# Optimization experiments

Hardware: AMD Instinct MI355X
Metric: run time of the kernel (lower is better)

The kernel has to match this reference:

```python
import jax, jax.numpy as jnp
import numpy as np

B, T, C, H = 4, 1024, 1024, 16
D = C // H  # head_size = 64
F = 4 * C   # ffn hidden


def _ln(x, g, b, eps=1e-5):
    m = x.mean(-1, keepdims=True)
    v = ((x - m) ** 2).mean(-1, keepdims=True)
    return (x - m) * jax.lax.rsqrt(v + eps) * g + b


def setup_inputs() -> dict:
    key = jax.random.key(0)
    ks = jax.random.split(key, 12)
    w = lambda k, shape: (jax.random.normal(k, shape, jnp.float32) * 0.02)
    return dict(
        x=jax.random.normal(ks[0], (B, T, C), jnp.float32),
        padding_mask=(jax.random.randint(ks[1], (B, T), 0, 2) == 1),
        Wq=w(ks[2], (H, C, D)),
        Wk=w(ks[3], (H, C, D)),
        Wv=w(ks[4], (H, C, D)),
        Wo=w(ks[5], (C, C)),
        bo=jnp.zeros((C,), jnp.float32),
        ln1_g=jnp.ones((C,), jnp.float32),
        ln1_b=jnp.zeros((C,), jnp.float32),
        ln2_g=jnp.ones((C,), jnp.float32),
        ln2_b=jnp.zeros((C,), jnp.float32),
        W1=w(ks[6], (C, F)),
        b1=jnp.zeros((F,), jnp.float32),
        W2=w(ks[7], (F, C)),
        b2=jnp.zeros((C,), jnp.float32),
    )


def reference(x, padding_mask, Wq, Wk, Wv, Wo, bo, ln1_g, ln1_b, ln2_g, ln2_b, W1, b1, W2, b2):
    Bn, Tn, Cn = x.shape
    h = _ln(x, ln1_g, ln1_b)
    # per-head q/k/v projections (no bias), vectorized over heads
    q = jnp.einsum('btc,hcd->bhtd', h, Wq)
    k = jnp.einsum('btc,hcd->bhtd', h, Wk)
    v = jnp.einsum('btc,hcd->bhtd', h, Wv)
    # NOTE: faithful to source, scale uses full n_embed C, not head_size
    wei = jnp.einsum('bhtd,bhsd->bhts', q, k) * (Cn ** -0.5)
    causal = jnp.tril(jnp.ones((Tn, Tn), bool))
    wei = jnp.where(causal[None, None], wei, -jnp.inf)
    # padding mask applied after causal, with -1e9 (as in source)
    wei = jnp.where(padding_mask[:, None, None, :], jnp.float32(-1e9), wei)
    att = jax.nn.softmax(wei, axis=-1)  # dropout is identity (eval)
    out = jnp.einsum('bhts,bhsd->bhtd', att, v)
    out = out.transpose(0, 2, 1, 3).reshape(Bn, Tn, Cn)  # concat heads
    out = out @ Wo + bo  # output projection
    # NOTE: no residual connections in the source TransformerBlock
    h2 = _ln(out, ln2_g, ln2_b)
    return jax.nn.relu(h2 @ W1 + b1) @ W2 + b2
```

## Files before the change

kernel.cpp:

```cpp
#include <hip/hip_runtime.h>
#include <hip/hip_bf16.h>
#include <math.h>

constexpr int kB = 4;
constexpr int kT = 1024;
constexpr int kC = 1024;
constexpr int kH = 16;
constexpr int kD = 64;
constexpr int kF = 4096;
constexpr int kBT = kB * kT;
constexpr int kSplit = 2;

typedef __attribute__((ext_vector_type(8))) short short8;
typedef __attribute__((ext_vector_type(4))) float f32x4;

__device__ __forceinline__ unsigned short f2bf(float f) {
    __hip_bfloat16 h = __float2bfloat16(f);
    return __builtin_bit_cast(unsigned short, h);
}
__device__ __forceinline__ float bf2f(unsigned short u) {
    return __bfloat162float(__builtin_bit_cast(__hip_bfloat16, u));
}


__global__ __launch_bounds__(256) void ln_bf16_kernel(const float* __restrict__ x,
                                                      const float* __restrict__ g,
                                                      const float* __restrict__ bta,
                                                      unsigned short* __restrict__ out) {
    int row = blockIdx.x;
    int t = threadIdx.x;
    float4 xv = ((const float4*)(x + (size_t)row * kC))[t];
    float s  = xv.x + xv.y + xv.z + xv.w;
    float sq = xv.x * xv.x + xv.y * xv.y + xv.z * xv.z + xv.w * xv.w;
    #pragma unroll
    for (int off = 32; off; off >>= 1) {
        s  += __shfl_xor(s, off);
        sq += __shfl_xor(sq, off);
    }
    __shared__ float sb[8];
    int wid = t >> 6, lane = t & 63;
    if (lane == 0) { sb[wid] = s; sb[4 + wid] = sq; }
    __syncthreads();
    s  = sb[0] + sb[1] + sb[2] + sb[3];
    sq = sb[4] + sb[5] + sb[6] + sb[7];
    float mean = s * (1.0f / kC);
    float var  = sq * (1.0f / kC) - mean * mean;
    float rs = rsqrtf(var + 1e-5f);
    float4 gv = ((const float4*)g)[t];
    float4 bv = ((const float4*)bta)[t];
    ushort4 o;
    o.x = f2bf((xv.x - mean) * rs * gv.x + bv.x);
    o.y = f2bf((xv.y - mean) * rs * gv.y + bv.y);
    o.z = f2bf((xv.z - mean) * rs * gv.z + bv.z);
    o.w = f2bf((xv.w - mean) * rs * gv.w + bv.w);
    *(ushort4*)(out + (size_t)row * kC + t * 4) = o;
}

__global__ __launch_bounds__(256) void transpose_w_kernel(const float* __restrict__ src,
                                                          unsigned short* __restrict__ dst,
                                                          int R, int C) {
    __shared__ float tile[64][65];
    src += (size_t)blockIdx.z * R * C;
    dst += (size_t)blockIdx.z * R * C;
    int r0 = blockIdx.x * 64, c0 = blockIdx.y * 64;
    int tid = threadIdx.x;
    int tr = tid >> 4, tc4 = (tid & 15) * 4;
    #pragma unroll
    for (int p = 0; p < 4; p++) {
        float4 v = *(const float4*)(src + (size_t)(r0 + tr + p * 16) * C + c0 + tc4);
        tile[tr + p * 16][tc4 + 0] = v.x;
        tile[tr + p * 16][tc4 + 1] = v.y;
        tile[tr + p * 16][tc4 + 2] = v.z;
        tile[tr + p * 16][tc4 + 3] = v.w;
    }
    __syncthreads();
    #pragma unroll
    for (int p = 0; p < 4; p++) {
        int c = tr + p * 16;
        ushort4 o;
        o.x = f2bf(tile[tc4 + 0][c]);
        o.y = f2bf(tile[tc4 + 1][c]);
        o.z = f2bf(tile[tc4 + 2][c]);
        o.w = f2bf(tile[tc4 + 3][c]);
        *(ushort4*)(dst + (size_t)(c0 + c) * R + r0 + tc4) = o;
    }
}

__global__ __launch_bounds__(256) void transpose_v_kernel(const unsigned short* __restrict__ qkv,
                                                          unsigned short* __restrict__ vt) {
    __shared__ unsigned short tile[64][68];
    int bh = blockIdx.y, b = bh >> 4, h = bh & 15;
    int t0 = blockIdx.x * 64;
    int tid = threadIdx.x;
    int tr = tid >> 4, tc4 = (tid & 15) * 4;
    #pragma unroll
    for (int p = 0; p < 4; p++) {
        int t = t0 + tr + p * 16;
        ushort4 v = *(const ushort4*)(qkv + ((size_t)(b * kT + t)) * 3072 + 2048 + h * 64 + tc4);
        *(ushort4*)&tile[tr + p * 16][tc4] = v;
    }
    __syncthreads();
    #pragma unroll
    for (int p = 0; p < 4; p++) {
        int d = tr + p * 16;
        ushort4 o;
        o.x = tile[tc4 + 0][d];
        o.y = tile[tc4 + 1][d];
        o.z = tile[tc4 + 2][d];
        o.w = tile[tc4 + 3][d];
        *(ushort4*)(vt + ((size_t)(bh * 64 + d)) * kT + t0 + tc4) = o;
    }
}

__global__ __launch_bounds__(256) void padscan_kernel(const int* __restrict__ pad,
                                                      int* __restrict__ npad,
                                                      int* __restrict__ fu) {
    int b = blockIdx.x, tid = threadIdx.x;
    int cnt = 0, f = kT;
    for (int t = tid; t < kT; t += 256) {
        int p = pad[b * kT + t];
        cnt += p;
        if (!p) f = min(f, t);
    }
    __shared__ int sc[256], sf[256];
    sc[tid] = cnt; sf[tid] = f;
    __syncthreads();
    for (int o = 128; o; o >>= 1) {
        if (tid < o) { sc[tid] += sc[tid + o]; sf[tid] = min(sf[tid], sf[tid + o]); }
        __syncthreads();
    }
    if (tid == 0) { npad[b] = sc[0]; fu[b] = sf[0]; }
}

__global__ __launch_bounds__(256) void meanv_kernel(const unsigned short* __restrict__ vt,
                                                    const int* __restrict__ pad,
                                                    const int* __restrict__ npad,
                                                    float* __restrict__ meanv) {
    int bh = blockIdx.x, b = bh >> 4;
    int tid = threadIdx.x, d = tid >> 2, seg = tid & 3;
    const unsigned short* row = vt + ((size_t)bh * 64 + d) * kT + seg * 256;
    const int* pr = pad + b * kT + seg * 256;
    float s = 0.f;
    for (int t = 0; t < 256; ++t)
        if (pr[t]) s += bf2f(row[t]);
    __shared__ float red[256];
    red[tid] = s;
    __syncthreads();
    if (seg == 0) {
        float tot = red[tid] + red[tid + 1] + red[tid + 2] + red[tid + 3];
        int np = npad[b];
        meanv[bh * 64 + d] = np > 0 ? tot / (float)np : 0.f;
    }
}

__global__ __launch_bounds__(256) void fixup_kernel(unsigned short* __restrict__ attnb,
                                                    const float* __restrict__ meanv,
                                                    const int* __restrict__ fu) {
    int b = blockIdx.x, tid = threadIdx.x;
    int f = fu[b];
    int c = tid * 4;
    ushort4 u;
    u.x = f2bf(meanv[b * kC + c + 0]);
    u.y = f2bf(meanv[b * kC + c + 1]);
    u.z = f2bf(meanv[b * kC + c + 2]);
    u.w = f2bf(meanv[b * kC + c + 3]);
    for (int t = 0; t < f; ++t)
        *(ushort4*)(attnb + ((size_t)(b * kT + t)) * kC + c) = u;
}

__global__ __launch_bounds__(256) void attn_partial(const unsigned short* __restrict__ qkv,
                                                    const unsigned short* __restrict__ vt,
                                                    const int* __restrict__ pad,
                                                    unsigned short* __restrict__ Opart,
                                                    float* __restrict__ Mpart,
                                                    float* __restrict__ Lpart) {
    __shared__ __align__(16) unsigned short Ks[64][72];
    __shared__ __align__(16) unsigned short Vs[64][72];
    __shared__ __align__(16) unsigned short Ps[4][16][72];
    const int tid = threadIdx.x;
    const int x = blockIdx.x, bh = blockIdx.y, j = blockIdx.z;
    const int b = bh >> 4, h = bh & 15;
    const int wv = tid >> 6, lane = tid & 63;
    const int lm = lane & 15, lk = lane >> 4;
    const int srow = tid >> 2, scol = (tid & 3) * 16;

    const int qrow = x * 64 + wv * 16 + lm;
    const size_t qoff = ((size_t)(b * kT + qrow)) * 3072 + h * 64 + lk * 8;
    short8 bq0 = *(const short8*)(qkv + qoff);
    short8 bq1 = *(const short8*)(qkv + qoff + 32);

    const unsigned short* kbase = qkv + ((size_t)(b * kT + srow)) * 3072 + 1024 + h * 64 + scol;
    const unsigned short* vbase = vt + ((size_t)(bh * 64 + srow)) * kT + scol;

    f32x4 o[4];
    #pragma unroll
    for (int dt = 0; dt < 4; dt++) o[dt] = (f32x4){0.f, 0.f, 0.f, 0.f};
    float m_i = -__builtin_inff(), l_i = 0.f;

    short8 kp0 = *(const short8*)(kbase + (size_t)(j * 64) * 3072);
    short8 kp1 = *(const short8*)(kbase + (size_t)(j * 64) * 3072 + 8);
    short8 vp0 = *(const short8*)(vbase + j * 64);
    short8 vp1 = *(const short8*)(vbase + j * 64 + 8);

    for (int c = j; c <= x; c += kSplit) {
        const int s0 = c * 64;
        *(short8*)&Ks[srow][scol] = kp0;
        *(short8*)&Ks[srow][scol + 8] = kp1;
        *(short8*)&Vs[srow][scol] = vp0;
        *(short8*)&Vs[srow][scol + 8] = vp1;
        __syncthreads();
        if (c + kSplit <= x) {
            const int sn = (c + kSplit) * 64;
            kp0 = *(const short8*)(kbase + (size_t)sn * 3072);
            kp1 = *(const short8*)(kbase + (size_t)sn * 3072 + 8);
            vp0 = *(const short8*)(vbase + sn);
            vp1 = *(const short8*)(vbase + sn + 8);
        }
        float xs[16];
        #pragma unroll
        for (int g = 0; g < 4; g++) {
            short8 ka0 = *(const short8*)&Ks[g * 16 + lm][lk * 8];
            short8 ka1 = *(const short8*)&Ks[g * 16 + lm][32 + lk * 8];
            f32x4 sc = (f32x4){0.f, 0.f, 0.f, 0.f};
            sc = __builtin_amdgcn_mfma_f32_16x16x32_bf16(ka0, bq0, sc, 0, 0, 0);
            sc = __builtin_amdgcn_mfma_f32_16x16x32_bf16(ka1, bq1, sc, 0, 0, 0);
            int sbase = s0 + g * 16 + lk * 4;
            int4 pv = *(const int4*)(pad + b * kT + sbase);
            int pa[4] = {pv.x, pv.y, pv.z, pv.w};
            #pragma unroll
            for (int r = 0; r < 4; r++) {
                float v = sc[r] * 0.03125f;
                if (sbase + r > qrow) v = -__builtin_inff();
                if (pa[r]) v = -1e9f;
                xs[g * 4 + r] = v;
            }
        }
        float mt = xs[0];
        #pragma unroll
        for (int i = 1; i < 16; i++) mt = fmaxf(mt, xs[i]);
        mt = fmaxf(mt, __shfl_xor(mt, 16));
        mt = fmaxf(mt, __shfl_xor(mt, 32));
        float mn = fmaxf(m_i, mt);
        float alpha = __expf(m_i - mn);
        float p[16], rs = 0.f;
        #pragma unroll
        for (int i = 0; i < 16; i++) { p[i] = __expf(xs[i] - mn); rs += p[i]; }
        rs += __shfl_xor(rs, 16);
        rs += __shfl_xor(rs, 32);
        l_i = l_i * alpha + rs;
        m_i = mn;
        #pragma unroll
        for (int g = 0; g < 4; g++) {
            ushort4 u;
            u.x = f2bf(p[g * 4 + 0]); u.y = f2bf(p[g * 4 + 1]);
            u.z = f2bf(p[g * 4 + 2]); u.w = f2bf(p[g * 4 + 3]);
            *(ushort4*)&Ps[wv][lm][g * 16 + lk * 4] = u;
        }
        float ar0 = __shfl(alpha, lk * 4 + 0);
        float ar1 = __shfl(alpha, lk * 4 + 1);
        float ar2 = __shfl(alpha, lk * 4 + 2);
        float ar3 = __shfl(alpha, lk * 4 + 3);
        #pragma unroll
        for (int dt = 0; dt < 4; dt++) {
            o[dt][0] *= ar0; o[dt][1] *= ar1; o[dt][2] *= ar2; o[dt][3] *= ar3;
        }
        short8 ap0 = *(const short8*)&Ps[wv][lm][lk * 8];
        short8 ap1 = *(const short8*)&Ps[wv][lm][32 + lk * 8];
        #pragma unroll
        for (int dt = 0; dt < 4; dt++) {
            short8 bv0 = *(const short8*)&Vs[dt * 16 + lm][lk * 8];
            short8 bv1 = *(const short8*)&Vs[dt * 16 + lm][32 + lk * 8];
            o[dt] = __builtin_amdgcn_mfma_f32_16x16x32_bf16(ap0, bv0, o[dt], 0, 0, 0);
            o[dt] = __builtin_amdgcn_mfma_f32_16x16x32_bf16(ap1, bv1, o[dt], 0, 0, 0);
        }
        __syncthreads();
    }
    const size_t base = ((size_t)(bh * kSplit + j)) * kT;
    if (lk == 0) {
        Mpart[base + qrow] = m_i;
        Lpart[base + qrow] = l_i;
    }
    #pragma unroll
    for (int dt = 0; dt < 4; dt++)
        #pragma unroll
        for (int r = 0; r < 4; r++) {
            int q = x * 64 + wv * 16 + lk * 4 + r;
            Opart[(base + q) * kD + dt * 16 + lm] = f2bf(o[dt][r]);
        }
}

__global__ __launch_bounds__(256) void attn_merge(const unsigned short* __restrict__ Opart,
                                                  const float* __restrict__ Mpart,
                                                  const float* __restrict__ Lpart,
                                                  unsigned short* __restrict__ attnb) {
    const int xq = blockIdx.x, bh = blockIdx.y;
    const int b = bh >> 4, h = bh & 15;
    const int tid = threadIdx.x;
    const int qo = tid >> 4, d4 = (tid & 15) * 4;
    #pragma unroll
    for (int pass = 0; pass < 4; pass++) {
        int q = xq * 64 + pass * 16 + qo;
        float m[kSplit], l[kSplit];
        float mstar = -__builtin_inff();
        #pragma unroll
        for (int jj = 0; jj < kSplit; jj++) {
            size_t base = ((size_t)(bh * kSplit + jj)) * kT + q;
            m[jj] = Mpart[base];
            l[jj] = Lpart[base];
            if (l[jj] > 0.f) mstar = fmaxf(mstar, m[jj]);
        }
        float acc0 = 0.f, acc1 = 0.f, acc2 = 0.f, acc3 = 0.f, L = 0.f;
        #pragma unroll
        for (int jj = 0; jj < kSplit; jj++) {
            if (l[jj] > 0.f) {
                float wgt = __expf(m[jj] - mstar);
                L += wgt * l[jj];
                ushort4 ov = *(const ushort4*)&Opart[(((size_t)(bh * kSplit + jj)) * kT + q) * kD + d4];
                acc0 += wgt * bf2f(ov.x);
                acc1 += wgt * bf2f(ov.y);
                acc2 += wgt * bf2f(ov.z);
                acc3 += wgt * bf2f(ov.w);
            }
        }
        float inv = 1.0f / L;
        ushort4 r;
        r.x = f2bf(acc0 * inv); r.y = f2bf(acc1 * inv);
        r.z = f2bf(acc2 * inv); r.w = f2bf(acc3 * inv);
        *(ushort4*)&attnb[((size_t)(b * kT + q)) * kC + h * 64 + d4] = r;
    }
}

template<int TM, int TN>
__global__ __launch_bounds__(256) void gemm_bt(const unsigned short* __restrict__ A,
                                               const unsigned short* __restrict__ Bt,
                                               const float* __restrict__ bias,
                                               float* __restrict__ Cf,
                                               unsigned short* __restrict__ Cb,
                                               int N, int K, int relu) {
    constexpr int AI = TM / 32, BJ = TN / 32;
    constexpr int TPRA = 256 / TM, TPRB = 256 / TN;
    constexpr int ACH = 64 / TPRA / 8, BCH = 64 / TPRB / 8;
    __shared__ __align__(16) unsigned short As[TM][72];
    __shared__ __align__(16) unsigned short Bs[TN][72];
    const int tid = threadIdx.x;
    const int wv = tid >> 6, lane = tid & 63;
    const int lm = lane & 15, lk = lane >> 4;
    const int arow = tid / TPRA, acb = (tid % TPRA) * (64 / TPRA);
    const int brow = tid / TPRB, bcb = (tid % TPRB) * (64 / TPRB);
    const int bm = blockIdx.y * TM, bn = blockIdx.x * TN;
    const int wm = (wv >> 1) * (TM / 2), wn = (wv & 1) * (TN / 2);
    f32x4 acc[AI][BJ];
    #pragma unroll
    for (int i = 0; i < AI; i++)
        #pragma unroll
        for (int j = 0; j < BJ; j++) acc[i][j] = (f32x4){0.f, 0.f, 0.f, 0.f};

    const unsigned short* Ap = A + (size_t)(bm + arow) * K + acb;
    const unsigned short* Bp = Bt + (size_t)(bn + brow) * K + bcb;
    short8 rA[ACH], rB[BCH];
    #pragma unroll
    for (int i = 0; i < ACH; i++) rA[i] = *(const short8*)(Ap + i * 8);
    #pragma unroll
    for (int i = 0; i < BCH; i++) rB[i] = *(const short8*)(Bp + i * 8);

    for (int k0 = 0; k0 < K; k0 += 64) {
        #pragma unroll
        for (int i = 0; i < ACH; i++)
            *(short8*)&As[arow][acb + i * 8] = rA[i];
        #pragma unroll
        for (int i = 0; i < BCH; i++)
            *(short8*)&Bs[brow][bcb + i * 8] = rB[i];
        __syncthreads();
        if (k0 + 64 < K) {
            #pragma unroll
            for (int i = 0; i < ACH; i++) rA[i] = *(const short8*)(Ap + k0 + 64 + i * 8);
            #pragma unroll
            for (int i = 0; i < BCH; i++) rB[i] = *(const short8*)(Bp + k0 + 64 + i * 8);
        }
        #pragma unroll
        for (int kk = 0; kk < 2; kk++) {
            short8 a[AI], bfr[BJ];
            #pragma unroll
            for (int i = 0; i < AI; i++)
                a[i] = *(const short8*)&As[wm + i * 16 + lm][kk * 32 + lk * 8];
            #pragma unroll
            for (int j = 0; j < BJ; j++)
                bfr[j] = *(const short8*)&Bs[wn + j * 16 + lm][kk * 32 + lk * 8];
            #pragma unroll
            for (int i = 0; i < AI; i++)
                #pragma unroll
                for (int j = 0; j < BJ; j++)
                    acc[i][j] = __builtin_amdgcn_mfma_f32_16x16x32_bf16(a[i], bfr[j], acc[i][j], 0, 0, 0);
        }
        __syncthreads();
    }
    #pragma unroll
    for (int j = 0; j < BJ; j++) {
        int col = bn + wn + j * 16 + lm;
        float bj = bias ? bias[col] : 0.f;
        #pragma unroll
        for (int i = 0; i < AI; i++) {
            #pragma unroll
            for (int r = 0; r < 4; r++) {
                int row = bm + wm + i * 16 + lk * 4 + r;
                float v = acc[i][j][r] + bj;
                if (relu) v = fmaxf(v, 0.f);
                if (Cf) Cf[(size_t)row * N + col] = v;
                else    Cb[(size_t)row * N + col] = f2bf(v);
            }
        }
    }
}

extern "C" void kernel_launch(void* const* d_in, const int* in_sizes, int n_in,
                              void* d_out, int out_size, void* d_ws, size_t ws_size,
                              hipStream_t stream) {
    (void)in_sizes; (void)n_in; (void)out_size; (void)ws_size;
    const float* x    = (const float*)d_in[0];
    const int*   pad  = (const int*)d_in[1];
    const float* Wq   = (const float*)d_in[2];
    const float* Wk   = (const float*)d_in[3];
    const float* Wv   = (const float*)d_in[4];
    const float* Wo   = (const float*)d_in[5];
    const float* bo   = (const float*)d_in[6];
    const float* ln1g = (const float*)d_in[7];
    const float* ln1b = (const float*)d_in[8];
    const float* ln2g = (const float*)d_in[9];
    const float* ln2b = (const float*)d_in[10];
    const float* W1   = (const float*)d_in[11];
    const float* b1   = (const float*)d_in[12];
    const float* W2   = (const float*)d_in[13];
    const float* b2   = (const float*)d_in[14];
    float* out = (float*)d_out;
    char* w = (char*)d_ws;

    constexpr size_t MB = 1024 * 1024;
    unsigned short* qkv   = (unsigned short*)(w + 0);
    float*          proj  = (float*)(w + 0);
    unsigned short* h2    = (unsigned short*)(w + 16 * MB);
    unsigned short* vt    = (unsigned short*)(w + 24 * MB);
    unsigned short* attnb = (unsigned short*)(w + 32 * MB);
    unsigned short* w1t   = (unsigned short*)(w + 40 * MB);
    unsigned short* w2t   = (unsigned short*)(w + 48 * MB);
    unsigned short* wot   = (unsigned short*)(w + 56 * MB);
    float*          meanv = (float*)(w + 58 * MB);
    int*            npad  = (int*)(w + 58 * MB + 65536);
    int*            fu    = (int*)(w + 58 * MB + 65536 + 64);
    unsigned short* h     = (unsigned short*)(w + 59 * MB);
    unsigned short* wqkvt = (unsigned short*)(w + 67 * MB);
    unsigned short* Opart = (unsigned short*)(w + 59 * MB);
    unsigned short* ffn1  = (unsigned short*)(w + 59 * MB);
    float*          Mpart = (float*)(w + 91 * MB);
    float*          Lpart = (float*)(w + 91 * MB + 512 * 1024);

    transpose_w_kernel<<<dim3(16, 1, 16), 256, 0, stream>>>(Wq, wqkvt,               kC, kD);
    transpose_w_kernel<<<dim3(16, 1, 16), 256, 0, stream>>>(Wk, wqkvt + 1024 * 1024, kC, kD);
    transpose_w_kernel<<<dim3(16, 1, 16), 256, 0, stream>>>(Wv, wqkvt + 2048 * 1024, kC, kD);
    transpose_w_kernel<<<dim3(16, 16, 1), 256, 0, stream>>>(Wo, wot, kC, kC);
    transpose_w_kernel<<<dim3(16, 64, 1), 256, 0, stream>>>(W1, w1t, kC, kF);
    transpose_w_kernel<<<dim3(64, 16, 1), 256, 0, stream>>>(W2, w2t, kF, kC);

    ln_bf16_kernel<<<kBT, 256, 0, stream>>>(x, ln1g, ln1b, h);
    gemm_bt<128, 128><<<dim3(24, 32), 256, 0, stream>>>(h, wqkvt, nullptr, nullptr, qkv,
                                                        3072, kC, 0);
    transpose_v_kernel<<<dim3(16, 64), 256, 0, stream>>>(qkv, vt);
    padscan_kernel<<<kB, 256, 0, stream>>>(pad, npad, fu);
    meanv_kernel<<<kB * kH, 256, 0, stream>>>(vt, pad, npad, meanv);
    attn_partial<<<dim3(16, 64, kSplit), 256, 0, stream>>>(qkv, vt, pad, Opart, Mpart, Lpart);
    attn_merge<<<dim3(16, 64), 256, 0, stream>>>(Opart, Mpart, Lpart, attnb);
    fixup_kernel<<<kB, 256, 0, stream>>>(attnb, meanv, fu);
    gemm_bt<128, 64><<<dim3(16, 32), 256, 0, stream>>>(attnb, wot, bo, proj, nullptr,
                                                       kC, kC, 0);
    ln_bf16_kernel<<<kBT, 256, 0, stream>>>(proj, ln2g, ln2b, h2);
    gemm_bt<128, 128><<<dim3(32, 32), 256, 0, stream>>>(h2, w1t, b1, nullptr, ffn1,
                                                        kF, kC, 1);
    gemm_bt<128, 64><<<dim3(16, 32), 256, 0, stream>>>(ffn1, w2t, b2, out, nullptr,
                                                       kC, kF, 0);
}
```

Baseline: 414.2 us.

## Merge weight transposes, fold padscan/fixup into meanv/merge, double-buffer GEMM LDS

All six weight-transpose launches become one kernel with a flat block index. The pad scan moves into meanv_kernel, and the fully-padded-row fixup moves into attn_merge, which cuts three launches and a serial fixup kernel. The GEMM now uses a K-tile of 32 with double-buffered LDS and one barrier per step, so loads overlap MFMA. In exchange, each GEMM step does half as much MFMA work per barrier, and meanv repeats the pad reduction in every head block.

```diff
diff --git a/kernel.cpp b/kernel.cpp
--- a/kernel.cpp
+++ b/kernel.cpp
@@ -56,13 +56,10 @@
     *(ushort4*)(out + (size_t)row * kC + t * 4) = o;
 }
 
-__global__ __launch_bounds__(256) void transpose_w_kernel(const float* __restrict__ src,
-                                                          unsigned short* __restrict__ dst,
-                                                          int R, int C) {
-    __shared__ float tile[64][65];
-    src += (size_t)blockIdx.z * R * C;
-    dst += (size_t)blockIdx.z * R * C;
-    int r0 = blockIdx.x * 64, c0 = blockIdx.y * 64;
+__device__ __forceinline__ void tile_tr(const float* __restrict__ src,
+                                        unsigned short* __restrict__ dst,
+                                        int R, int C, int r0, int c0,
+                                        float (*tile)[65]) {
     int tid = threadIdx.x;
     int tr = tid >> 4, tc4 = (tid & 15) * 4;
     #pragma unroll
@@ -86,6 +83,36 @@
     }
 }
 
+__global__ __launch_bounds__(256) void transpose_all(const float* __restrict__ Wq,
+                                                     const float* __restrict__ Wk,
+                                                     const float* __restrict__ Wv,
+                                                     const float* __restrict__ Wo,
+                                                     const float* __restrict__ W1,
+                                                     const float* __restrict__ W2,
+                                                     unsigned short* __restrict__ wqkvt,
+                                                     unsigned short* __restrict__ wot,
+                                                     unsigned short* __restrict__ w1t,
+                                                     unsigned short* __restrict__ w2t) {
+    __shared__ float tile[64][65];
+    int id = blockIdx.x;
+    if (id < 768) {
+        int wsel = id >> 8, t = id & 255;
+        int z = t >> 4, xq = t & 15;
+        const float* s = (wsel == 0 ? Wq : wsel == 1 ? Wk : Wv) + (size_t)z * 65536;
+        tile_tr(s, wqkvt + (size_t)wsel * 1048576 + (size_t)z * 65536,
+                1024, 64, xq * 64, 0, tile);
+    } else if (id < 1024) {
+        int t = id - 768;
+        tile_tr(Wo, wot, 1024, 1024, (t & 15) * 64, (t >> 4) * 64, tile);
+    } else if (id < 2048) {
+        int t = id - 1024;
+        tile_tr(W1, w1t, 1024, 4096, (t & 15) * 64, (t >> 4) * 64, tile);
+    } else {
+        int t = id - 2048;
+        tile_tr(W2, w2t, 4096, 1024, (t & 63) * 64, (t >> 6) * 64, tile);
+    }
+}
+
 __global__ __launch_bounds__(256) void transpose_v_kernel(const unsigned short* __restrict__ qkv,
                                                           unsigned short* __restrict__ vt) {
     __shared__ unsigned short tile[64][68];
@@ -112,60 +139,53 @@
     }
 }
 
-__global__ __launch_bounds__(256) void padscan_kernel(const int* __restrict__ pad,
-                                                      int* __restrict__ npad,
-                                                      int* __restrict__ fu) {
-    int b = blockIdx.x, tid = threadIdx.x;
-    int cnt = 0, f = kT;
-    for (int t = tid; t < kT; t += 256) {
-        int p = pad[b * kT + t];
-        cnt += p;
-        if (!p) f = min(f, t);
-    }
-    __shared__ int sc[256], sf[256];
-    sc[tid] = cnt; sf[tid] = f;
-    __syncthreads();
-    for (int o = 128; o; o >>= 1) {
-        if (tid < o) { sc[tid] += sc[tid + o]; sf[tid] = min(sf[tid], sf[tid + o]); }
-        __syncthreads();
-    }
-    if (tid == 0) { npad[b] = sc[0]; fu[b] = sf[0]; }
-}
-
 __global__ __launch_bounds__(256) void meanv_kernel(const unsigned short* __restrict__ vt,
                                                     const int* __restrict__ pad,
-                                                    const int* __restrict__ npad,
-                                                    float* __restrict__ meanv) {
+                                                    float* __restrict__ meanv,
+                                                    int* __restrict__ fu) {
     int bh = blockIdx.x, b = bh >> 4;
-    int tid = threadIdx.x, d = tid >> 2, seg = tid & 3;
+    int tid = threadIdx.x;
+    __shared__ char padc[kT];
+    __shared__ int ri[256];
+    __shared__ float rf[256];
+    int4 pv = *(const int4*)(pad + b * kT + tid * 4);
+    padc[tid * 4 + 0] = (char)pv.x;
+    padc[tid * 4 + 1] = (char)pv.y;
+    padc[tid * 4 + 2] = (char)pv.z;
+    padc[tid * 4 + 3] = (char)pv.w;
+    int cnt = pv.x + pv.y + pv.z + pv.w;
+    int f = kT;
+    if (!pv.w) f = tid * 4 + 3;
+    if (!pv.z) f = tid * 4 + 2;
+    if (!pv.y) f = tid * 4 + 1;
+    if (!pv.x) f = tid * 4 + 0;
+    ri[tid] = f;
+    __syncthreads();
+    for (int o = 128; o; o >>= 1) {
+        if (tid < o) ri[tid] = min(ri[tid], ri[tid + o]);
+        __syncthreads();
+    }
+    int fu_s = ri[0];
+    __syncthreads();
+    ri[tid] = cnt;
+    __syncthreads();
+    for (int o = 128; o; o >>= 1) {
+        if (tid < o) ri[tid] += ri[tid + o];
+        __syncthreads();
+    }
+    int np = ri[0];
+    int d = tid >> 2, seg = tid & 3;
     const unsigned short* row = vt + ((size_t)bh * 64 + d) * kT + seg * 256;
-    const int* pr = pad + b * kT + seg * 256;
     float s = 0.f;
     for (int t = 0; t < 256; ++t)
-        if (pr[t]) s += bf2f(row[t]);
-    __shared__ float red[256];
-    red[tid] = s;
+        if (padc[seg * 256 + t]) s += bf2f(row[t]);
+    rf[tid] = s;
     __syncthreads();
     if (seg == 0) {
-        float tot = red[tid] + red[tid + 1] + red[tid + 2] + red[tid + 3];
-        int np = npad[b];
+        float tot = rf[tid] + rf[tid + 1] + rf[tid + 2] + rf[tid + 3];
         meanv[bh * 64 + d] = np > 0 ? tot / (float)np : 0.f;
     }
-}
-
-__global__ __launch_bounds__(256) void fixup_kernel(unsigned short* __restrict__ attnb,
-                                                    const float* __restrict__ meanv,
-                                                    const int* __restrict__ fu) {
-    int b = blockIdx.x, tid = threadIdx.x;
-    int f = fu[b];
-    int c = tid * 4;
-    ushort4 u;
-    u.x = f2bf(meanv[b * kC + c + 0]);
-    u.y = f2bf(meanv[b * kC + c + 1]);
-    u.z = f2bf(meanv[b * kC + c + 2]);
-    u.w = f2bf(meanv[b * kC + c + 3]);
-    for (int t = 0; t < f; ++t)
-        *(ushort4*)(attnb + ((size_t)(b * kT + t)) * kC + c) = u;
+    if (tid == 0 && (bh & 15) == 0) fu[b] = fu_s;
 }
 
 __global__ __launch_bounds__(256) void attn_partial(const unsigned short* __restrict__ qkv,
@@ -292,40 +312,50 @@
 __global__ __launch_bounds__(256) void attn_merge(const unsigned short* __restrict__ Opart,
                                                   const float* __restrict__ Mpart,
                                                   const float* __restrict__ Lpart,
+                                                  const float* __restrict__ meanv,
+                                                  const int* __restrict__ fu,
                                                   unsigned short* __restrict__ attnb) {
     const int xq = blockIdx.x, bh = blockIdx.y;
     const int b = bh >> 4, h = bh & 15;
     const int tid = threadIdx.x;
     const int qo = tid >> 4, d4 = (tid & 15) * 4;
+    const int f = fu[b];
     #pragma unroll
     for (int pass = 0; pass < 4; pass++) {
         int q = xq * 64 + pass * 16 + qo;
-        float m[kSplit], l[kSplit];
-        float mstar = -__builtin_inff();
-        #pragma unroll
-        for (int jj = 0; jj < kSplit; jj++) {
-            size_t base = ((size_t)(bh * kSplit + jj)) * kT + q;
-            m[jj] = Mpart[base];
-            l[jj] = Lpart[base];
-            if (l[jj] > 0.f) mstar = fmaxf(mstar, m[jj]);
-        }
-        float acc0 = 0.f, acc1 = 0.f, acc2 = 0.f, acc3 = 0.f, L = 0.f;
-        #pragma unroll
-        for (int jj = 0; jj < kSplit; jj++) {
-            if (l[jj] > 0.f) {
-                float wgt = __expf(m[jj] - mstar);
-                L += wgt * l[jj];
-                ushort4 ov = *(const ushort4*)&Opart[(((size_t)(bh * kSplit + jj)) * kT + q) * kD + d4];
-                acc0 += wgt * bf2f(ov.x);
-                acc1 += wgt * bf2f(ov.y);
-                acc2 += wgt * bf2f(ov.z);
-                acc3 += wgt * bf2f(ov.w);
+        ushort4 r;
+        if (q < f) {
+            r.x = f2bf(meanv[bh * 64 + d4 + 0]);
+            r.y = f2bf(meanv[bh * 64 + d4 + 1]);
+            r.z = f2bf(meanv[bh * 64 + d4 + 2]);
+            r.w = f2bf(meanv[bh * 64 + d4 + 3]);
+        } else {
+            float m[kSplit], l[kSplit];
+            float mstar = -__builtin_inff();
+            #pragma unroll
+            for (int jj = 0; jj < kSplit; jj++) {
+                size_t base = ((size_t)(bh * kSplit + jj)) * kT + q;
+                m[jj] = Mpart[base];
+                l[jj] = Lpart[base];
+                if (l[jj] > 0.f) mstar = fmaxf(mstar, m[jj]);
             }
-        }
-        float inv = 1.0f / L;
-        ushort4 r;
-        r.x = f2bf(acc0 * inv); r.y = f2bf(acc1 * inv);
-        r.z = f2bf(acc2 * inv); r.w = f2bf(acc3 * inv);
+            float acc0 = 0.f, acc1 = 0.f, acc2 = 0.f, acc3 = 0.f, L = 0.f;
+            #pragma unroll
+            for (int jj = 0; jj < kSplit; jj++) {
+                if (l[jj] > 0.f) {
+                    float wgt = __expf(m[jj] - mstar);
+                    L += wgt * l[jj];
+                    ushort4 ov = *(const ushort4*)&Opart[(((size_t)(bh * kSplit + jj)) * kT + q) * kD + d4];
+                    acc0 += wgt * bf2f(ov.x);
+                    acc1 += wgt * bf2f(ov.y);
+                    acc2 += wgt * bf2f(ov.z);
+                    acc3 += wgt * bf2f(ov.w);
+                }
+            }
+            float inv = 1.0f / L;
+            r.x = f2bf(acc0 * inv); r.y = f2bf(acc1 * inv);
+            r.z = f2bf(acc2 * inv); r.w = f2bf(acc3 * inv);
+        }
         *(ushort4*)&attnb[((size_t)(b * kT + q)) * kC + h * 64 + d4] = r;
     }
 }
@@ -339,14 +369,14 @@
                                                int N, int K, int relu) {
     constexpr int AI = TM / 32, BJ = TN / 32;
     constexpr int TPRA = 256 / TM, TPRB = 256 / TN;
-    constexpr int ACH = 64 / TPRA / 8, BCH = 64 / TPRB / 8;
-    __shared__ __align__(16) unsigned short As[TM][72];
-    __shared__ __align__(16) unsigned short Bs[TN][72];
+    constexpr int ACH = 32 / TPRA / 8, BCH = 32 / TPRB / 8;
+    __shared__ __align__(16) unsigned short As[2][TM][40];
+    __shared__ __align__(16) unsigned short Bs[2][TN][40];
     const int tid = threadIdx.x;
     const int wv = tid >> 6, lane = tid & 63;
     const int lm = lane & 15, lk = lane >> 4;
-    const int arow = tid / TPRA, acb = (tid % TPRA) * (64 / TPRA);
-    const int brow = tid / TPRB, bcb = (tid % TPRB) * (64 / TPRB);
+    const int arow = tid / TPRA, acb = (tid % TPRA) * (32 / TPRA);
+    const int brow = tid / TPRB, bcb = (tid % TPRB) * (32 / TPRB);
     const int bm = blockIdx.y * TM, bn = blockIdx.x * TN;
     const int wm = (wv >> 1) * (TM / 2), wn = (wv & 1) * (TN / 2);
     f32x4 acc[AI][BJ];
@@ -362,35 +392,38 @@
     for (int i = 0; i < ACH; i++) rA[i] = *(const short8*)(Ap + i * 8);
     #pragma unroll
     for (int i = 0; i < BCH; i++) rB[i] = *(const short8*)(Bp + i * 8);
-
-    for (int k0 = 0; k0 < K; k0 += 64) {
-        #pragma unroll
-        for (int i = 0; i < ACH; i++)
-            *(short8*)&As[arow][acb + i * 8] = rA[i];
-        #pragma unroll
-        for (int i = 0; i < BCH; i++)
-            *(short8*)&Bs[brow][bcb + i * 8] = rB[i];
-        __syncthreads();
-        if (k0 + 64 < K) {
-            #pragma unroll
-            for (int i = 0; i < ACH; i++) rA[i] = *(const short8*)(Ap + k0 + 64 + i * 8);
-            #pragma unroll
-            for (int i = 0; i < BCH; i++) rB[i] = *(const short8*)(Bp + k0 + 64 + i * 8);
-        }
-        #pragma unroll
-        for (int kk = 0; kk < 2; kk++) {
-            short8 a[AI], bfr[BJ];
-            #pragma unroll
-            for (int i = 0; i < AI; i++)
-                a[i] = *(const short8*)&As[wm + i * 16 + lm][kk * 32 + lk * 8];
+    #pragma unroll
+    for (int i = 0; i < ACH; i++) *(short8*)&As[0][arow][acb + i * 8] = rA[i];
+    #pragma unroll
+    for (int i = 0; i < BCH; i++) *(short8*)&Bs[0][brow][bcb + i * 8] = rB[i];
+    __syncthreads();
+
+    for (int k0 = 0; k0 < K; k0 += 32) {
+        const int cur = (k0 >> 5) & 1;
+        const bool more = (k0 + 32 < K);
+        if (more) {
+            #pragma unroll
+            for (int i = 0; i < ACH; i++) rA[i] = *(const short8*)(Ap + k0 + 32 + i * 8);
+            #pragma unroll
+            for (int i = 0; i < BCH; i++) rB[i] = *(const short8*)(Bp + k0 + 32 + i * 8);
+        }
+        short8 a[AI], bfr[BJ];
+        #pragma unroll
+        for (int i = 0; i < AI; i++)
+            a[i] = *(const short8*)&As[cur][wm + i * 16 + lm][lk * 8];
+        #pragma unroll
+        for (int j = 0; j < BJ; j++)
+            bfr[j] = *(const short8*)&Bs[cur][wn + j * 16 + lm][lk * 8];
+        #pragma unroll
+        for (int i = 0; i < AI; i++)
             #pragma unroll
             for (int j = 0; j < BJ; j++)
-                bfr[j] = *(const short8*)&Bs[wn + j * 16 + lm][kk * 32 + lk * 8];
-            #pragma unroll
-            for (int i = 0; i < AI; i++)
-                #pragma unroll
-                for (int j = 0; j < BJ; j++)
-                    acc[i][j] = __builtin_amdgcn_mfma_f32_16x16x32_bf16(a[i], bfr[j], acc[i][j], 0, 0, 0);
+                acc[i][j] = __builtin_amdgcn_mfma_f32_16x16x32_bf16(a[i], bfr[j], acc[i][j], 0, 0, 0);
+        if (more) {
+            #pragma unroll
+            for (int i = 0; i < ACH; i++) *(short8*)&As[cur ^ 1][arow][acb + i * 8] = rA[i];
+            #pragma unroll
+            for (int i = 0; i < BCH; i++) *(short8*)&Bs[cur ^ 1][brow][bcb + i * 8] = rB[i];
         }
         __syncthreads();
     }
@@ -444,8 +477,7 @@
     unsigned short* w2t   = (unsigned short*)(w + 48 * MB);
     unsigned short* wot   = (unsigned short*)(w + 56 * MB);
     float*          meanv = (float*)(w + 58 * MB);
-    int*            npad  = (int*)(w + 58 * MB + 65536);
-    int*            fu    = (int*)(w + 58 * MB + 65536 + 64);
+    int*            fu    = (int*)(w + 58 * MB + 65536);
     unsigned short* h     = (unsigned short*)(w + 59 * MB);
     unsigned short* wqkvt = (unsigned short*)(w + 67 * MB);
     unsigned short* Opart = (unsigned short*)(w + 59 * MB);
@@ -453,22 +485,15 @@
     float*          Mpart = (float*)(w + 91 * MB);
     float*          Lpart = (float*)(w + 91 * MB + 512 * 1024);
 
-    transpose_w_kernel<<<dim3(16, 1, 16), 256, 0, stream>>>(Wq, wqkvt,               kC, kD);
-    transpose_w_kernel<<<dim3(16, 1, 16), 256, 0, stream>>>(Wk, wqkvt + 1024 * 1024, kC, kD);
-    transpose_w_kernel<<<dim3(16, 1, 16), 256, 0, stream>>>(Wv, wqkvt + 2048 * 1024, kC, kD);
-    transpose_w_kernel<<<dim3(16, 16, 1), 256, 0, stream>>>(Wo, wot, kC, kC);
-    transpose_w_kernel<<<dim3(16, 64, 1), 256, 0, stream>>>(W1, w1t, kC, kF);
-    transpose_w_kernel<<<dim3(64, 16, 1), 256, 0, stream>>>(W2, w2t, kF, kC);
-
+    transpose_all<<<3072, 256, 0, stream>>>(Wq, Wk, Wv, Wo, W1, W2,
+                                            wqkvt, wot, w1t, w2t);
     ln_bf16_kernel<<<kBT, 256, 0, stream>>>(x, ln1g, ln1b, h);
     gemm_bt<128, 128><<<dim3(24, 32), 256, 0, stream>>>(h, wqkvt, nullptr, nullptr, qkv,
                                                         3072, kC, 0);
     transpose_v_kernel<<<dim3(16, 64), 256, 0, stream>>>(qkv, vt);
-    padscan_kernel<<<kB, 256, 0, stream>>>(pad, npad, fu);
-    meanv_kernel<<<kB * kH, 256, 0, stream>>>(vt, pad, npad, meanv);
+    meanv_kernel<<<kB * kH, 256, 0, stream>>>(vt, pad, meanv, fu);
     attn_partial<<<dim3(16, 64, kSplit), 256, 0, stream>>>(qkv, vt, pad, Opart, Mpart, Lpart);
-    attn_merge<<<dim3(16, 64), 256, 0, stream>>>(Opart, Mpart, Lpart, attnb);
-    fixup_kernel<<<kB, 256, 0, stream>>>(attnb, meanv, fu);
+    attn_merge<<<dim3(16, 64), 256, 0, stream>>>(Opart, Mpart, Lpart, meanv, fu, attnb);
     gemm_bt<128, 64><<<dim3(16, 32), 256, 0, stream>>>(attnb, wot, bo, proj, nullptr,
                                                        kC, kC, 0);
     ln_bf16_kernel<<<kBT, 256, 0, stream>>>(proj, ln2g, ln2b, h2);
```

New measurement: 422.0 us. No clear change (+1.9%).
